# Optimization experiments

Hardware: AMD Instinct MI355X
Metric: run time of the kernel (lower is better)

## Reference

```python
import jax, jax.numpy as jnp
import numpy as np


def setup_inputs() -> dict:
    key = jax.random.key(0)
    k1, k2 = jax.random.split(key)
    x = jax.random.normal(k1, (8, 2500, 100), dtype=jnp.float32)          # [B, L, E]
    label_feature = jax.random.normal(k2, (8922, 100), dtype=jnp.float32)  # [N, E]
    return {"x": x, "label_feature": label_feature}


def reference(x, label_feature):
    # scores: [B, N, L] = label_feature @ x^T (broadcast query over batch), unscaled
    scores = jnp.einsum("ne,ble->bnl", label_feature, x)
    alpha = jax.nn.softmax(scores, axis=2)  # softmax over sequence length
    # m: [B, N, E] = alpha @ x
    m = jnp.einsum("bnl,ble->bne", alpha, x)
    return m
```

## Files before the change

kernel.cpp:

```cpp
#include <hip/hip_runtime.h>
#include <math.h>
#include <stdint.h>

typedef __attribute__((ext_vector_type(8))) _Float16 half8;
typedef __attribute__((ext_vector_type(16))) float f32x16;
typedef __attribute__((ext_vector_type(4))) uint32_t uint4v;

constexpr int Bb = 8, Ll = 2500, Ee = 100, Nn = 8922;
constexpr int LP = 2560, EP = 128, NP = 8960;
constexpr int VE = 112;
constexpr int LT = 64;
constexpr int NTILES = LP / LT;
constexpr int NTB = 128;

constexpr size_t SZ_LF = (size_t)NP * EP * 2;
constexpr size_t SZ_XW = (size_t)Bb * LP * EP * 2;
constexpr size_t SZ_XT = (size_t)Bb * VE * LP * 2;
constexpr size_t OFF_XW = SZ_LF;
constexpr size_t OFF_XT = OFF_XW + SZ_XW;
constexpr size_t WS_NEED = OFF_XT + SZ_XT;

__device__ __forceinline__ void gload16(const void* g, void* l) {
    __builtin_amdgcn_global_load_lds(
        (const __attribute__((address_space(1))) uint32_t*)g,
        (__attribute__((address_space(3))) uint32_t*)l, 16, 0, 0);
}

__global__ __launch_bounds__(256)
void prep_all(const float* __restrict__ x, const float* __restrict__ lf,
              uint32_t* __restrict__ dlf, uint32_t* __restrict__ dxw,
              uint16_t* __restrict__ dxt) {
    if (blockIdx.y == Bb) {
        for (int idx = blockIdx.x * 256 + threadIdx.x; idx < NP * 64; idx += 40 * 256) {
            int n = idx >> 6, ep = idx & 63;
            int e0 = 2 * ep, e1 = e0 + 1;
            float f0 = (n < Nn && e0 < Ee) ? lf[(size_t)n * Ee + e0] : 0.f;
            float f1 = (n < Nn && e1 < Ee) ? lf[(size_t)n * Ee + e1] : (e1 == 127 ? 1.0f : 0.f);
            union { _Float16 h[2]; uint32_t u; } cv;
            cv.h[0] = (_Float16)f0; cv.h[1] = (_Float16)f1;
            dlf[idx] = cv.u;
        }
        return;
    }
    __shared__ float lx[64][101];
    const int l0 = blockIdx.x * 64;
    const int b  = blockIdx.y;
    for (int i = threadIdx.x; i < 64 * Ee; i += 256) {
        int ll = i / Ee, e = i - ll * Ee;
        int l = l0 + ll;
        lx[ll][e] = (l < Ll) ? x[((size_t)b * Ll + l) * Ee + e] : 0.f;
    }
    __syncthreads();
    for (int i = threadIdx.x; i < 64 * 64; i += 256) {
        int row = i >> 6, ep = i & 63;
        int l = l0 + row;
        int e0 = 2 * ep, e1 = e0 + 1;
        float f0 = (e0 < Ee) ? lx[row][e0] : 0.f;
        float f1;
        if (e1 < Ee)        f1 = lx[row][e1];
        else if (e1 == 127) f1 = (l < Ll) ? 0.f : -20000.f;
        else                f1 = 0.f;
        union { _Float16 h[2]; uint32_t u; } cv;
        cv.h[0] = (_Float16)f0; cv.h[1] = (_Float16)f1;
        int boff = (4 * ep) ^ ((row & 15) << 4);
        dxw[((size_t)b * LP + l) * 64 + (boff >> 2)] = cv.u;
    }
    for (int i = threadIdx.x; i < VE * 64; i += 256) {
        int e = i >> 6, ll = i & 63;
        float v = (e < Ee) ? lx[ll][e] : 0.f;
        uint32_t boff = (uint32_t)((2 * ll) ^ ((e & 7) << 4));
        union { _Float16 h; uint16_t u; } cv; cv.h = (_Float16)v;
        dxt[((size_t)b * VE + e) * LP + l0 + (boff >> 1)] = cv.u;
    }
}

__global__ __launch_bounds__(256, 3)
void cwa_mfma(const uint16_t* __restrict__ lf16, const uint16_t* __restrict__ xw,
              const uint16_t* __restrict__ xt, float* __restrict__ out) {
    __shared__ __align__(128) char smem[49152];
    const int tid = threadIdx.x, lane = tid & 63, w = tid >> 6;
    const int r31 = lane & 31, hi = lane >> 5;
    const int o = blockIdx.x;
    const int b = o & 7, xb = o >> 3;
    const int n_base = xb * NTB + w * 32;

    const char* xwb = (const char*)(xw + (size_t)b * LP * EP);
    const char* xtb = (const char*)(xt + (size_t)b * VE * LP);

    auto stage_k = [&](int t, int p) {
        const char* kg = xwb + (size_t)t * (LT * EP * 2);
        char* kbuf = smem + p * 16384;
#pragma unroll
        for (int i = 0; i < 4; i++) {
            int off = i * 4096 + tid * 16;
            gload16(kg + off, kbuf + off);
        }
    };
    auto stage_v = [&](int t) {
        const char* vg = xtb + (size_t)t * (LT * 2);
        char* vbuf = smem + 32768;
#pragma unroll
        for (int i = 0; i < 3; i++) {
            int u = i * 256 + tid;
            gload16(vg + (size_t)(u >> 3) * (LP * 2) + (u & 7) * 16, vbuf + u * 16);
        }
        if (tid < 128) {
            int u = 768 + tid;
            gload16(vg + (size_t)(u >> 3) * (LP * 2) + (u & 7) * 16, vbuf + u * 16);
        }
    };

    stage_k(0, 0);
    stage_v(0);

    half8 qf[8];
    {
        const uint16_t* qr = lf16 + (size_t)(n_base + r31) * EP + 8 * hi;
#pragma unroll
        for (int ks = 0; ks < 8; ks++) qf[ks] = *(const half8*)(qr + 16 * ks);
    }
    asm volatile("s_waitcnt vmcnt(0)" ::: "memory");
    __syncthreads();
    stage_k(1, 1);

    f32x16 oacc[4];
#pragma unroll
    for (int eb = 0; eb < 4; eb++)
#pragma unroll
        for (int r = 0; r < 16; r++) oacc[eb][r] = 0.f;
    float m_i = -INFINITY, s_i = 0.f;

    const char* vb = smem + 32768;
    const int kkey = r31 & 15;
    const int vkey = r31 & 7;

    for (int t = 0; t < NTILES; t++) {
        const int p = t & 1;
        const char* kb = smem + p * 16384;

        f32x16 sacc[2];
#pragma unroll
        for (int lb = 0; lb < 2; lb++)
#pragma unroll
            for (int r = 0; r < 16; r++) sacc[lb][r] = 0.f;
#pragma unroll
        for (int lb = 0; lb < 2; lb++) {
            const char* kr = kb + (32 * lb + r31) * 256;
#pragma unroll
            for (int ks = 0; ks < 8; ks++) {
                half8 kf = *(const half8*)(kr + (((2 * ks + hi) ^ kkey) << 4));
                sacc[lb] = __builtin_amdgcn_mfma_f32_32x32x16_f16(kf, qf[ks], sacc[lb], 0, 0, 0);
            }
        }

        float tmv = -INFINITY;
#pragma unroll
        for (int lb = 0; lb < 2; lb++)
#pragma unroll
            for (int r = 0; r < 16; r++) tmv = fmaxf(tmv, sacc[lb][r]);
        tmv = fmaxf(tmv, __shfl_xor(tmv, 32, 64));

        if (!__all(tmv <= m_i + 8.f)) {
            const float mn = fmaxf(m_i, tmv);
            const float sc = __expf(m_i - mn);
            m_i = mn;
            s_i *= sc;
#pragma unroll
            for (int r = 0; r < 16; r++) {
                float scr = __shfl(sc, (r & 3) + 8 * (r >> 2) + 4 * hi, 64);
#pragma unroll
                for (int eb = 0; eb < 4; eb++) oacc[eb][r] *= scr;
            }
        }

        half8 pa[4];
        float ts = 0.f;
#pragma unroll
        for (int lb = 0; lb < 2; lb++) {
            uint32_t c[8], xch[8];
#pragma unroll
            for (int i = 0; i < 8; i++) {
                float p0 = __expf(sacc[lb][2 * i]     - m_i);
                float p1 = __expf(sacc[lb][2 * i + 1] - m_i);
                ts += p0 + p1;
                c[i] = __builtin_bit_cast(uint32_t, __builtin_amdgcn_cvt_pkrtz(p0, p1));
            }
#pragma unroll
            for (int i = 0; i < 8; i++) xch[i] = __shfl_xor(c[i], 32, 64);
            uint4v wa = {hi ? xch[2] : c[0], hi ? xch[3] : c[1],
                         hi ? c[2] : xch[0], hi ? c[3] : xch[1]};
            uint4v wb2 = {hi ? xch[6] : c[4], hi ? xch[7] : c[5],
                          hi ? c[6] : xch[4], hi ? c[7] : xch[5]};
            pa[2 * lb]     = __builtin_bit_cast(half8, wa);
            pa[2 * lb + 1] = __builtin_bit_cast(half8, wb2);
        }
        ts += __shfl_xor(ts, 32, 64);
        s_i += ts;

#pragma unroll
        for (int eb = 0; eb < 4; eb++) {
            const char* vr = vb + (32 * eb + r31) * 128;
#pragma unroll
            for (int kk = 0; kk < 4; kk++) {
                half8 vf = *(const half8*)(vr + (((2 * kk + hi) ^ vkey) << 4));
                oacc[eb] = __builtin_amdgcn_mfma_f32_32x32x16_f16(pa[kk], vf, oacc[eb], 0, 0, 0);
            }
        }

        __syncthreads();
        const int tv = min(t + 1, NTILES - 1);
        const int tk = min(t + 2, NTILES - 1);
        stage_v(tv);
        stage_k(tk, p);
        asm volatile("s_waitcnt vmcnt(4)" ::: "memory");
        __syncthreads();
    }

    const float inv = 1.0f / s_i;
#pragma unroll
    for (int r = 0; r < 16; r++) {
        const int nrow = (r & 3) + 8 * (r >> 2) + 4 * hi;
        const float invr = __shfl(inv, nrow, 64);
        const int n = n_base + nrow;
        if (n < Nn) {
            float* orow = out + ((size_t)b * Nn + n) * Ee;
            orow[r31]      = oacc[0][r] * invr;
            orow[32 + r31] = oacc[1][r] * invr;
            orow[64 + r31] = oacc[2][r] * invr;
            if (r31 < 4) orow[96 + r31] = oacc[3][r] * invr;
        }
    }
}

constexpr int FNT = 16, FLT = 64, FLTP = 65;
__global__ __launch_bounds__(256)
void cwa_fwd(const float* __restrict__ x, const float* __restrict__ lf,
             float* __restrict__ out) {
    __shared__ float q[FNT][Ee];
    __shared__ float xts[Ee][FLTP];
    __shared__ float pl[FNT][FLT];
    const int tid = threadIdx.x, lane = tid & 63, w = tid >> 6;
    const int b = blockIdx.y, n0 = blockIdx.x * FNT;
    for (int idx = tid; idx < FNT * Ee; idx += 256) {
        int nl = idx / Ee, e = idx - nl * Ee;
        int n = n0 + nl;
        q[nl][e] = (n < Nn) ? lf[n * Ee + e] : 0.0f;
    }
    float m_i[4], s_i[4], a0[4], a1[4];
#pragma unroll
    for (int i = 0; i < 4; i++) { m_i[i] = -INFINITY; s_i[i] = 0.f; a0[i] = 0.f; a1[i] = 0.f; }
    const float* xb = x + (size_t)b * Ll * Ee;
    const bool hi_ok = lane < (Ee - 64);
    for (int l0 = 0; l0 < Ll; l0 += FLT) {
        const int nrows = min(FLT, Ll - l0);
        __syncthreads();
        for (int idx = tid; idx < FLT * (Ee / 4); idx += 256) {
            int r = idx / (Ee / 4), c4 = idx - r * (Ee / 4);
            float4 v = make_float4(0.f, 0.f, 0.f, 0.f);
            if (r < nrows) v = *reinterpret_cast<const float4*>(xb + (size_t)(l0 + r) * Ee + c4 * 4);
            xts[c4 * 4 + 0][r] = v.x; xts[c4 * 4 + 1][r] = v.y;
            xts[c4 * 4 + 2][r] = v.z; xts[c4 * 4 + 3][r] = v.w;
        }
        __syncthreads();
        float sc[4] = {0.f, 0.f, 0.f, 0.f};
        for (int e = 0; e < Ee; e++) {
            float xv = xts[e][lane];
#pragma unroll
            for (int i = 0; i < 4; i++) sc[i] = fmaf(q[4 * w + i][e], xv, sc[i]);
        }
        const bool valid = lane < nrows;
#pragma unroll
        for (int i = 0; i < 4; i++) {
            float s = valid ? sc[i] : -INFINITY;
            float tmv = s;
#pragma unroll
            for (int msk = 32; msk >= 1; msk >>= 1) tmv = fmaxf(tmv, __shfl_xor(tmv, msk, 64));
            float mn = fmaxf(m_i[i], tmv);
            float pp = __expf(s - mn);
            float sm = pp;
#pragma unroll
            for (int msk = 32; msk >= 1; msk >>= 1) sm += __shfl_xor(sm, msk, 64);
            float scl = __expf(m_i[i] - mn);
            s_i[i] = s_i[i] * scl + sm; m_i[i] = mn;
            a0[i] *= scl; a1[i] *= scl;
            pl[4 * w + i][lane] = pp;
        }
        __syncthreads();
#pragma unroll 4
        for (int l = 0; l < FLT; l++) {
            float xv0 = xts[lane][l];
            float xv1 = hi_ok ? xts[64 + lane][l] : 0.f;
#pragma unroll
            for (int i = 0; i < 4; i++) {
                float pv = pl[4 * w + i][l];
                a0[i] = fmaf(pv, xv0, a0[i]); a1[i] = fmaf(pv, xv1, a1[i]);
            }
        }
    }
#pragma unroll
    for (int i = 0; i < 4; i++) {
        int n = n0 + 4 * w + i;
        if (n >= Nn) continue;
        float inv = 1.0f / s_i[i];
        size_t base = ((size_t)b * Nn + n) * Ee;
        out[base + lane] = a0[i] * inv;
        if (hi_ok) out[base + 64 + lane] = a1[i] * inv;
    }
}

extern "C" void kernel_launch(void* const* d_in, const int* in_sizes, int n_in,
                              void* d_out, int out_size, void* d_ws, size_t ws_size,
                              hipStream_t stream) {
    const float* x  = (const float*)d_in[0];
    const float* lf = (const float*)d_in[1];
    float* out = (float*)d_out;
    if (ws_size >= WS_NEED) {
        uint32_t* dlf = (uint32_t*)d_ws;
        uint32_t* dxw = (uint32_t*)((char*)d_ws + OFF_XW);
        uint16_t* dxt = (uint16_t*)((char*)d_ws + OFF_XT);
        prep_all<<<dim3(LP / 64, Bb + 1), 256, 0, stream>>>(x, lf, dlf, dxw, dxt);
        cwa_mfma<<<dim3((NP / NTB) * Bb), 256, 0, stream>>>(
            (const uint16_t*)dlf, (const uint16_t*)dxw, dxt, out);
    } else {
        dim3 grid((Nn + FNT - 1) / FNT, Bb);
        cwa_fwd<<<grid, dim3(256), 0, stream>>>(x, lf, out);
    }
}
```

Before: 234.7 us.

## Double-buffer V tiles and issue next-tile prefetch at loop start

Adds a second V buffer in shared memory and restructures the pipeline. K and V for tile t+1 are now prefetched at the top of each iteration, which removes the mid-loop barrier and the partial-wait scheme. The change also raises wave priority around the MFMA sections and splits the max and sum reductions into trees to shorten dependency chains. Shared memory grows and launch bounds drop from 3 to 2 blocks per CU, so occupancy may fall. Prefetch depth also shrinks from two K tiles ahead to one.

```diff
diff --git a/kernel.cpp b/kernel.cpp
--- a/kernel.cpp
+++ b/kernel.cpp
@@ -74,10 +74,10 @@
     }
 }
 
-__global__ __launch_bounds__(256, 3)
+__global__ __launch_bounds__(256, 2)
 void cwa_mfma(const uint16_t* __restrict__ lf16, const uint16_t* __restrict__ xw,
               const uint16_t* __restrict__ xt, float* __restrict__ out) {
-    __shared__ __align__(128) char smem[49152];
+    __shared__ __align__(128) char smem[61440];
     const int tid = threadIdx.x, lane = tid & 63, w = tid >> 6;
     const int r31 = lane & 31, hi = lane >> 5;
     const int o = blockIdx.x;
@@ -96,9 +96,9 @@
             gload16(kg + off, kbuf + off);
         }
     };
-    auto stage_v = [&](int t) {
+    auto stage_v = [&](int t, int p) {
         const char* vg = xtb + (size_t)t * (LT * 2);
-        char* vbuf = smem + 32768;
+        char* vbuf = smem + 32768 + p * 14336;
 #pragma unroll
         for (int i = 0; i < 3; i++) {
             int u = i * 256 + tid;
@@ -111,8 +111,7 @@
     };
 
     stage_k(0, 0);
-    stage_v(0);
-
+    stage_v(0, 0);
     half8 qf[8];
     {
         const uint16_t* qr = lf16 + (size_t)(n_base + r31) * EP + 8 * hi;
@@ -121,7 +120,6 @@
     }
     asm volatile("s_waitcnt vmcnt(0)" ::: "memory");
     __syncthreads();
-    stage_k(1, 1);
 
     f32x16 oacc[4];
 #pragma unroll
@@ -130,19 +128,25 @@
         for (int r = 0; r < 16; r++) oacc[eb][r] = 0.f;
     float m_i = -INFINITY, s_i = 0.f;
 
-    const char* vb = smem + 32768;
     const int kkey = r31 & 15;
     const int vkey = r31 & 7;
 
     for (int t = 0; t < NTILES; t++) {
         const int p = t & 1;
         const char* kb = smem + p * 16384;
+        const char* vb = smem + 32768 + p * 14336;
+
+        if (t + 1 < NTILES) {
+            stage_k(t + 1, p ^ 1);
+            stage_v(t + 1, p ^ 1);
+        }
 
         f32x16 sacc[2];
 #pragma unroll
         for (int lb = 0; lb < 2; lb++)
 #pragma unroll
             for (int r = 0; r < 16; r++) sacc[lb][r] = 0.f;
+        __builtin_amdgcn_s_setprio(1);
 #pragma unroll
         for (int lb = 0; lb < 2; lb++) {
             const char* kr = kb + (32 * lb + r31) * 256;
@@ -152,13 +156,22 @@
                 sacc[lb] = __builtin_amdgcn_mfma_f32_32x32x16_f16(kf, qf[ks], sacc[lb], 0, 0, 0);
             }
         }
-
-        float tmv = -INFINITY;
-#pragma unroll
-        for (int lb = 0; lb < 2; lb++)
-#pragma unroll
-            for (int r = 0; r < 16; r++) tmv = fmaxf(tmv, sacc[lb][r]);
-        tmv = fmaxf(tmv, __shfl_xor(tmv, 32, 64));
+        __builtin_amdgcn_s_setprio(0);
+
+        float tmv;
+        {
+            float v0 = fmaxf(fmaxf(sacc[0][0], sacc[0][1]), fmaxf(sacc[0][2], sacc[0][3]));
+            float v1 = fmaxf(fmaxf(sacc[0][4], sacc[0][5]), fmaxf(sacc[0][6], sacc[0][7]));
+            float v2 = fmaxf(fmaxf(sacc[0][8], sacc[0][9]), fmaxf(sacc[0][10], sacc[0][11]));
+            float v3 = fmaxf(fmaxf(sacc[0][12], sacc[0][13]), fmaxf(sacc[0][14], sacc[0][15]));
+            float v4 = fmaxf(fmaxf(sacc[1][0], sacc[1][1]), fmaxf(sacc[1][2], sacc[1][3]));
+            float v5 = fmaxf(fmaxf(sacc[1][4], sacc[1][5]), fmaxf(sacc[1][6], sacc[1][7]));
+            float v6 = fmaxf(fmaxf(sacc[1][8], sacc[1][9]), fmaxf(sacc[1][10], sacc[1][11]));
+            float v7 = fmaxf(fmaxf(sacc[1][12], sacc[1][13]), fmaxf(sacc[1][14], sacc[1][15]));
+            tmv = fmaxf(fmaxf(fmaxf(v0, v1), fmaxf(v2, v3)),
+                        fmaxf(fmaxf(v4, v5), fmaxf(v6, v7)));
+            tmv = fmaxf(tmv, __shfl_xor(tmv, 32, 64));
+        }
 
         if (!__all(tmv <= m_i + 8.f)) {
             const float mn = fmaxf(m_i, tmv);
@@ -174,7 +187,7 @@
         }
 
         half8 pa[4];
-        float ts = 0.f;
+        float ts0 = 0.f, ts1 = 0.f, ts2 = 0.f, ts3 = 0.f;
 #pragma unroll
         for (int lb = 0; lb < 2; lb++) {
             uint32_t c[8], xch[8];
@@ -182,7 +195,12 @@
             for (int i = 0; i < 8; i++) {
                 float p0 = __expf(sacc[lb][2 * i]     - m_i);
                 float p1 = __expf(sacc[lb][2 * i + 1] - m_i);
-                ts += p0 + p1;
+                switch (i & 3) {
+                    case 0: ts0 += p0 + p1; break;
+                    case 1: ts1 += p0 + p1; break;
+                    case 2: ts2 += p0 + p1; break;
+                    default: ts3 += p0 + p1; break;
+                }
                 c[i] = __builtin_bit_cast(uint32_t, __builtin_amdgcn_cvt_pkrtz(p0, p1));
             }
 #pragma unroll
@@ -194,9 +212,11 @@
             pa[2 * lb]     = __builtin_bit_cast(half8, wa);
             pa[2 * lb + 1] = __builtin_bit_cast(half8, wb2);
         }
+        float ts = (ts0 + ts1) + (ts2 + ts3);
         ts += __shfl_xor(ts, 32, 64);
         s_i += ts;
 
+        __builtin_amdgcn_s_setprio(1);
 #pragma unroll
         for (int eb = 0; eb < 4; eb++) {
             const char* vr = vb + (32 * eb + r31) * 128;
@@ -206,13 +226,9 @@
                 oacc[eb] = __builtin_amdgcn_mfma_f32_32x32x16_f16(pa[kk], vf, oacc[eb], 0, 0, 0);
             }
         }
-
-        __syncthreads();
-        const int tv = min(t + 1, NTILES - 1);
-        const int tk = min(t + 2, NTILES - 1);
-        stage_v(tv);
-        stage_k(tk, p);
-        asm volatile("s_waitcnt vmcnt(4)" ::: "memory");
+        __builtin_amdgcn_s_setprio(0);
+
+        asm volatile("s_waitcnt vmcnt(0)" ::: "memory");
         __syncthreads();
     }
 
```

Result: slower. 261.4 us (+11.4%).
